# Optimization experiments

Measured on AMD Instinct MI355X. Metric: run time of the kernel, lower is better.

## Reference

```python
import jax, jax.numpy as jnp
import numpy as np

B, RSS_DIM, N_LED, LED_FEAT, HEAD_DIM = 1024, 12, 2048, 8, 64


def _mlp(x, W1, b1, W2, b2):
    # two-layer MLP with ReLU hidden
    return jax.nn.relu(x @ W1 + b1) @ W2 + b2


def setup_inputs() -> dict:
    key = jax.random.key(0)
    ks = jax.random.split(key, 16)
    s = lambda fan_in: 1.0 / np.sqrt(fan_in)
    inp = {
        "rss_t": jax.random.uniform(ks[0], (B, RSS_DIM, 1), jnp.float32),
        "led_features": jax.random.normal(ks[1], (B, N_LED, LED_FEAT), jnp.float32),
        "led_positions": jax.random.normal(ks[2], (B, N_LED, 3), jnp.float32),
        "prev_pos": jax.random.normal(ks[3], (B, 3), jnp.float32),
        "freq_mask": jax.random.randint(ks[4], (RSS_DIM, N_LED), 0, 2, jnp.int32),
        # intensity_gate: Linear(1,16) -> ReLU -> Linear(16,1) -> Sigmoid
        "Wg1": jax.random.normal(ks[5], (1, 16), jnp.float32) * s(1),
        "bg1": jnp.zeros((16,), jnp.float32),
        "Wg2": jax.random.normal(ks[6], (16, 1), jnp.float32) * s(16),
        "bg2": jnp.zeros((1,), jnp.float32),
        # query_proj: Linear(1,32) -> ReLU -> Linear(32,64)
        "Wq1": jax.random.normal(ks[7], (1, 32), jnp.float32) * s(1),
        "bq1": jnp.zeros((32,), jnp.float32),
        "Wq2": jax.random.normal(ks[8], (32, HEAD_DIM), jnp.float32) * s(32),
        "bq2": jnp.zeros((HEAD_DIM,), jnp.float32),
        # key_proj: Linear(led_feat+3, 32) -> ReLU -> Linear(32, 64)
        "Wk1": jax.random.normal(ks[9], (LED_FEAT + 3, 32), jnp.float32) * s(LED_FEAT + 3),
        "bk1": jnp.zeros((32,), jnp.float32),
        "Wk2": jax.random.normal(ks[10], (32, HEAD_DIM), jnp.float32) * s(32),
        "bk2": jnp.zeros((HEAD_DIM,), jnp.float32),
        "sigma": jnp.asarray(0.5, jnp.float32),
    }
    return inp


def reference(rss_t, led_features, led_positions, prev_pos, freq_mask,
              Wg1, bg1, Wg2, bg2, Wq1, bq1, Wq2, bq2, Wk1, bk1, Wk2, bk2, sigma):
    # gated intensity filter on RSS channels
    hard_mask = (rss_t > 0.5).astype(rss_t.dtype)              # [B, R, 1]
    soft_gate = jax.nn.sigmoid(_mlp(rss_t, Wg1, bg1, Wg2, bg2))  # [B, R, 1]
    intensity_weight = hard_mask * soft_gate                    # [B, R, 1]
    masked_rss = rss_t * intensity_weight

    Q = _mlp(masked_rss, Wq1, bq1, Wq2, bq2)                    # [B, R, D]
    led_input = jnp.concatenate([led_features, led_positions], axis=-1)  # [B, N, F+3]
    K = _mlp(led_input, Wk1, bk1, Wk2, bk2)                     # [B, N, D]

    attn_scores = jnp.einsum("brd,bnd->brn", Q, K)              # [B, R, N]

    # near-field distance bias from previous position
    dist_sq = jnp.sum((prev_pos[:, None, :] - led_positions) ** 2, axis=-1)  # [B, N]
    near_field_bias = -dist_sq[:, None, :] / (2.0 * sigma ** 2)  # broadcast to [B, R, N]
    attn_scores = attn_scores + near_field_bias

    # hard frequency mask then softmax over LEDs
    neg = jnp.finfo(attn_scores.dtype).min
    attn_scores = jnp.where(freq_mask[None, :, :] == 0, neg, attn_scores)
    attn_weights = jax.nn.softmax(attn_scores, axis=-1)
    return attn_weights, intensity_weight[..., 0]
```

## Files before the change

kernel.cpp:

```cpp
#include <hip/hip_runtime.h>
#include <math.h>
#include <float.h>

#define B_ 1024
#define R_ 12
#define N_ 2048

typedef float floatx4 __attribute__((ext_vector_type(4)));

__global__ void __launch_bounds__(1024) const_kernel(
    const float* __restrict__ Wq2, const float* __restrict__ bq2,
    const float* __restrict__ Wk2, const float* __restrict__ bk2,
    const float* __restrict__ Wk1, const float* __restrict__ bk1,
    float* __restrict__ Mmat, float* __restrict__ uvec,
    float* __restrict__ vvec, float* __restrict__ k0p,
    float* __restrict__ WkT)
{
    const int t = threadIdx.x;
    const int i = t >> 5, j = t & 31;
    float m = 0.0f;
    for (int d = 0; d < 64; d++) m += Wq2[i * 64 + d] * Wk2[j * 64 + d];
    Mmat[t] = m;
    if (t < 32) {
        float v = 0.0f;
        for (int d = 0; d < 64; d++) v += Wk2[t * 64 + d] * bq2[d];
        vvec[t] = v;
    } else if (t < 64) {
        float u = 0.0f;
        for (int d = 0; d < 64; d++) u += Wq2[(t - 32) * 64 + d] * bk2[d];
        uvec[t - 32] = u;
    } else if (t == 64) {
        float k = 0.0f;
        for (int d = 0; d < 64; d++) k += bq2[d] * bk2[d];
        k0p[0] = k;
    }
    if (t < 384) {
        const int jj = t / 12, e = t - jj * 12;
        WkT[t] = (e < 11) ? Wk1[e * 32 + jj] : bk1[jj];
    }
}

__global__ void __launch_bounds__(256) prep_kernel(
    const float* __restrict__ rss,
    const float* __restrict__ Wg1, const float* __restrict__ bg1,
    const float* __restrict__ Wg2, const float* __restrict__ bg2,
    const float* __restrict__ Wq1, const float* __restrict__ bq1,
    const float* __restrict__ Mmat, const float* __restrict__ uvec,
    const float* __restrict__ vvec, const float* __restrict__ k0p,
    const int*   __restrict__ mask,
    float* __restrict__ qpT,
    float* __restrict__ cc,
    int*   __restrict__ maskbits,
    float* __restrict__ inten_out)
{
    const int gt = blockIdx.x * 256 + threadIdx.x;

    if (gt < N_) {
        int bits = 0;
#pragma unroll
        for (int r = 0; r < R_; r++) bits |= (mask[r * N_ + gt] != 0) << r;
        maskbits[gt] = bits;
    }

    if (gt >= B_ * R_) return;
    const int b = gt / 12, r = gt - b * 12;

    const float x = rss[gt];
    const float hard = (x > 0.5f) ? 1.0f : 0.0f;

    float s2 = bg2[0];
#pragma unroll
    for (int i = 0; i < 16; i++)
        s2 += fmaxf(x * Wg1[i] + bg1[i], 0.0f) * Wg2[i];
    const float gate = 1.0f / (1.0f + __expf(-s2));
    const float iw = hard * gate;
    const float xm = x * iw;

    const floatx4* vv = reinterpret_cast<const floatx4*>(vvec);
    floatx4 Q0 = vv[0], Q1 = vv[1], Q2 = vv[2], Q3 = vv[3];
    floatx4 Q4 = vv[4], Q5 = vv[5], Q6 = vv[6], Q7 = vv[7];
    float c = k0p[0];

#pragma unroll
    for (int i = 0; i < 32; i++) {
        const float h = fmaxf(xm * Wq1[i] + bq1[i], 0.0f);
        const floatx4* mr = reinterpret_cast<const floatx4*>(Mmat + i * 32);
        Q0 += h * mr[0]; Q1 += h * mr[1]; Q2 += h * mr[2]; Q3 += h * mr[3];
        Q4 += h * mr[4]; Q5 += h * mr[5]; Q6 += h * mr[6]; Q7 += h * mr[7];
        c  += h * uvec[i];
    }

    float* qb = qpT + (size_t)b * 384 + r;
#define STQ(k)                          \
    qb[(4 * k + 0) * 12] = Q##k.x;      \
    qb[(4 * k + 1) * 12] = Q##k.y;      \
    qb[(4 * k + 2) * 12] = Q##k.z;      \
    qb[(4 * k + 3) * 12] = Q##k.w;
    STQ(0) STQ(1) STQ(2) STQ(3) STQ(4) STQ(5) STQ(6) STQ(7)
#undef STQ

    cc[gt] = c;
    inten_out[gt] = iw;
}

__global__ void __launch_bounds__(512, 2) main_kernel(
    const float* __restrict__ ledf,
    const float* __restrict__ ledp,
    const float* __restrict__ prevp,
    const int*   __restrict__ maskbits,
    const float* __restrict__ WkT,
    const float* __restrict__ qpT,
    const float* __restrict__ cc,
    const float* __restrict__ sigp,
    float* __restrict__ out)
{
    const int b = blockIdx.x;
    const int tid = threadIdx.x;
    const int lane = tid & 63;
    const int wave = tid >> 6;
    const int n0 = tid * 4;

    __shared__ float sW[32 * 12];
    __shared__ float sQ[32 * 12];
    __shared__ float red[8 * 12];

    if (tid < 384) {
        sW[tid] = WkT[tid];
        sQ[tid] = qpT[(size_t)b * 384 + tid];
    }

    const float* __restrict__ ccb = cc + b * 12;
    const float sig = sigp[0];
    const float nfc = -0.5f / (sig * sig);
    const float p0 = prevp[b * 3 + 0];
    const float p1 = prevp[b * 3 + 1];
    const float p2 = prevp[b * 3 + 2];

    const floatx4* pf = reinterpret_cast<const floatx4*>(ledf + ((size_t)b * N_ + n0) * 8);
    const floatx4* pp4 = reinterpret_cast<const floatx4*>(ledp + ((size_t)b * N_ + n0) * 3);
    const floatx4 F0 = pf[0], F1 = pf[1], F2 = pf[2], F3 = pf[3];
    const floatx4 F4 = pf[4], F5 = pf[5], F6 = pf[6], F7 = pf[7];
    const floatx4 pa = pp4[0], pb = pp4[1], pc = pp4[2];
    const int4 mb = *reinterpret_cast<const int4*>(maskbits + n0);

    const floatx4 X0 = {F0.x, F2.x, F4.x, F6.x};
    const floatx4 X1 = {F0.y, F2.y, F4.y, F6.y};
    const floatx4 X2 = {F0.z, F2.z, F4.z, F6.z};
    const floatx4 X3 = {F0.w, F2.w, F4.w, F6.w};
    const floatx4 X4 = {F1.x, F3.x, F5.x, F7.x};
    const floatx4 X5 = {F1.y, F3.y, F5.y, F7.y};
    const floatx4 X6 = {F1.z, F3.z, F5.z, F7.z};
    const floatx4 X7 = {F1.w, F3.w, F5.w, F7.w};
    const floatx4 X8 = {pa.x, pa.w, pb.z, pc.y};
    const floatx4 X9 = {pa.y, pb.x, pb.w, pc.z};
    const floatx4 X10 = {pa.z, pb.y, pc.x, pc.w};

    const floatx4 DX = p0 - X8, DY = p1 - X9, DZ = p2 - X10;
    const floatx4 BIAS = nfc * (DX * DX + DY * DY + DZ * DZ);

#define FOR_R(OP) OP(0) OP(1) OP(2) OP(3) OP(4) OP(5) OP(6) OP(7) OP(8) OP(9) OP(10) OP(11)
#define INIT_R(r) floatx4 A##r = BIAS + ccb[r];
    FOR_R(INIT_R)

    __syncthreads();

#pragma unroll 4
    for (int j = 0; j < 32; j++) {
        const floatx4 w0 = *reinterpret_cast<const floatx4*>(&sW[j * 12]);
        const floatx4 w1 = *reinterpret_cast<const floatx4*>(&sW[j * 12 + 4]);
        const floatx4 w2 = *reinterpret_cast<const floatx4*>(&sW[j * 12 + 8]);
        const floatx4 q0 = *reinterpret_cast<const floatx4*>(&sQ[j * 12]);
        const floatx4 q1 = *reinterpret_cast<const floatx4*>(&sQ[j * 12 + 4]);
        const floatx4 q2 = *reinterpret_cast<const floatx4*>(&sQ[j * 12 + 8]);

        floatx4 H = {w2.w, w2.w, w2.w, w2.w};
        H += X0 * w0.x;  H += X1 * w0.y;  H += X2 * w0.z;  H += X3 * w0.w;
        H += X4 * w1.x;  H += X5 * w1.y;  H += X6 * w1.z;  H += X7 * w1.w;
        H += X8 * w2.x;  H += X9 * w2.y;  H += X10 * w2.z;
        H.x = fmaxf(H.x, 0.0f);
        H.y = fmaxf(H.y, 0.0f);
        H.z = fmaxf(H.z, 0.0f);
        H.w = fmaxf(H.w, 0.0f);

        A0 += H * q0.x;  A1 += H * q0.y;  A2  += H * q0.z;  A3  += H * q0.w;
        A4 += H * q1.x;  A5 += H * q1.y;  A6  += H * q1.z;  A7  += H * q1.w;
        A8 += H * q2.x;  A9 += H * q2.y;  A10 += H * q2.z;  A11 += H * q2.w;
    }

#define MASK_R(r)                                      \
    A##r.x = ((mb.x >> r) & 1) ? A##r.x : -FLT_MAX;    \
    A##r.y = ((mb.y >> r) & 1) ? A##r.y : -FLT_MAX;    \
    A##r.z = ((mb.z >> r) & 1) ? A##r.z : -FLT_MAX;    \
    A##r.w = ((mb.w >> r) & 1) ? A##r.w : -FLT_MAX;
    FOR_R(MASK_R)

#define WMAX_R(r) {                                                     \
    float v = fmaxf(fmaxf(A##r.x, A##r.y), fmaxf(A##r.z, A##r.w));      \
    _Pragma("unroll")                                                   \
    for (int off = 32; off >= 1; off >>= 1) v = fmaxf(v, __shfl_xor(v, off)); \
    if (lane == 0) red[wave * 12 + r] = v; }
    FOR_R(WMAX_R)
    __syncthreads();
#define FMAX_R(r) float M##r = red[r];                                  \
    { _Pragma("unroll")                                                 \
      for (int w = 1; w < 8; w++) M##r = fmaxf(M##r, red[w * 12 + r]); }
    FOR_R(FMAX_R)
    __syncthreads();

#define EXP_R(r) {                                                      \
    A##r.x = __expf(A##r.x - M##r); A##r.y = __expf(A##r.y - M##r);     \
    A##r.z = __expf(A##r.z - M##r); A##r.w = __expf(A##r.w - M##r);     \
    float v = (A##r.x + A##r.y) + (A##r.z + A##r.w);                    \
    _Pragma("unroll")                                                   \
    for (int off = 32; off >= 1; off >>= 1) v += __shfl_xor(v, off);    \
    if (lane == 0) red[wave * 12 + r] = v; }
    FOR_R(EXP_R)
    __syncthreads();
#define FSUM_R(r) float S##r = red[r];                                  \
    { _Pragma("unroll")                                                 \
      for (int w = 1; w < 8; w++) S##r += red[w * 12 + r]; }            \
    S##r = 1.0f / S##r;
    FOR_R(FSUM_R)

    float* outp = out + (size_t)b * R_ * N_ + n0;
#define STORE_R(r) {                                                    \
    floatx4 v = A##r * S##r;                                            \
    __builtin_nontemporal_store(v, reinterpret_cast<floatx4*>(outp + (size_t)r * N_)); }
    FOR_R(STORE_R)
}

extern "C" void kernel_launch(void* const* d_in, const int* in_sizes, int n_in,
                              void* d_out, int out_size, void* d_ws, size_t ws_size,
                              hipStream_t stream) {
    const float* rss  = (const float*)d_in[0];
    const float* ledf = (const float*)d_in[1];
    const float* ledp = (const float*)d_in[2];
    const float* prevp= (const float*)d_in[3];
    const int*   mask = (const int*)  d_in[4];
    const float* Wg1  = (const float*)d_in[5];
    const float* bg1  = (const float*)d_in[6];
    const float* Wg2  = (const float*)d_in[7];
    const float* bg2  = (const float*)d_in[8];
    const float* Wq1  = (const float*)d_in[9];
    const float* bq1  = (const float*)d_in[10];
    const float* Wq2  = (const float*)d_in[11];
    const float* bq2  = (const float*)d_in[12];
    const float* Wk1  = (const float*)d_in[13];
    const float* bk1  = (const float*)d_in[14];
    const float* Wk2  = (const float*)d_in[15];
    const float* bk2  = (const float*)d_in[16];
    const float* sigp = (const float*)d_in[17];

    float* out = (float*)d_out;
    float* inten = out + (size_t)B_ * R_ * N_;

    float* qpT      = (float*)d_ws;
    float* cc       = qpT + (size_t)B_ * 384;
    int*   maskbits = (int*)(cc + B_ * R_);
    float* Mmat     = (float*)(maskbits + N_);
    float* uvec     = Mmat + 1024;
    float* vvec     = uvec + 32;
    float* k0p      = vvec + 32;
    float* WkT      = k0p + 4;

    const_kernel<<<1, 1024, 0, stream>>>(Wq2, bq2, Wk2, bk2, Wk1, bk1,
                                         Mmat, uvec, vvec, k0p, WkT);

    prep_kernel<<<(B_ * R_ + 255) / 256, 256, 0, stream>>>(
        rss, Wg1, bg1, Wg2, bg2, Wq1, bq1,
        Mmat, uvec, vvec, k0p, mask, qpT, cc, maskbits, inten);

    main_kernel<<<B_, 512, 0, stream>>>(
        ledf, ledp, prevp, maskbits, WkT, qpT, cc, sigp, out);
}
```

Measured before the change: 293.4 us.

## Process two batches per block with 8 LEDs per thread and prefetch

The main kernel now uses 512 blocks of 256 threads. Each block handles batches b and b+512, and each thread covers 8 LEDs instead of 4. The second batch's LED feature and position loads are issued before the first batch's softmax and stores, so that global-load latency hides behind reduction work. In exchange, far fewer waves are resident, register pressure is much higher, and memory-latency hiding now depends on the explicit prefetch rather than occupancy.

```diff
diff --git a/kernel.cpp b/kernel.cpp
--- a/kernel.cpp
+++ b/kernel.cpp
@@ -92,10 +92,10 @@
 
     float* qb = qpT + (size_t)b * 384 + r;
 #define STQ(k)                          \
-    qb[(4 * k + 0) * 12] = Q##k.x;      \
-    qb[(4 * k + 1) * 12] = Q##k.y;      \
-    qb[(4 * k + 2) * 12] = Q##k.z;      \
-    qb[(4 * k + 3) * 12] = Q##k.w;
+    qb[(4 * k + 0) * 12] = Q##k .x;     \
+    qb[(4 * k + 1) * 12] = Q##k .y;     \
+    qb[(4 * k + 2) * 12] = Q##k .z;     \
+    qb[(4 * k + 3) * 12] = Q##k .w;
     STQ(0) STQ(1) STQ(2) STQ(3) STQ(4) STQ(5) STQ(6) STQ(7)
 #undef STQ
 
@@ -103,7 +103,121 @@
     inten_out[gt] = iw;
 }
 
-__global__ void __launch_bounds__(512, 2) main_kernel(
+#define FOR_R(OP) OP(0) OP(1) OP(2) OP(3) OP(4) OP(5) OP(6) OP(7) OP(8) OP(9) OP(10) OP(11)
+#define FOR_R2(OP, X) OP(0,X) OP(1,X) OP(2,X) OP(3,X) OP(4,X) OP(5,X) OP(6,X) OP(7,X) OP(8,X) OP(9,X) OP(10,X) OP(11,X)
+
+#define TRANS_BIAS(O, F, P, PX, PY, PZ)                                 \
+    const floatx4 O##A0 = {F##0 .x, F##2 .x, F##4 .x, F##6 .x};         \
+    const floatx4 O##A1 = {F##0 .y, F##2 .y, F##4 .y, F##6 .y};         \
+    const floatx4 O##A2 = {F##0 .z, F##2 .z, F##4 .z, F##6 .z};         \
+    const floatx4 O##A3 = {F##0 .w, F##2 .w, F##4 .w, F##6 .w};         \
+    const floatx4 O##A4 = {F##1 .x, F##3 .x, F##5 .x, F##7 .x};         \
+    const floatx4 O##A5 = {F##1 .y, F##3 .y, F##5 .y, F##7 .y};         \
+    const floatx4 O##A6 = {F##1 .z, F##3 .z, F##5 .z, F##7 .z};         \
+    const floatx4 O##A7 = {F##1 .w, F##3 .w, F##5 .w, F##7 .w};         \
+    const floatx4 O##A8 = {P##0 .x, P##0 .w, P##1 .z, P##2 .y};         \
+    const floatx4 O##A9 = {P##0 .y, P##1 .x, P##1 .w, P##2 .z};         \
+    const floatx4 O##A10 = {P##0 .z, P##1 .y, P##2 .x, P##2 .w};        \
+    const floatx4 O##B0 = {F##8 .x, F##10 .x, F##12 .x, F##14 .x};      \
+    const floatx4 O##B1 = {F##8 .y, F##10 .y, F##12 .y, F##14 .y};      \
+    const floatx4 O##B2 = {F##8 .z, F##10 .z, F##12 .z, F##14 .z};      \
+    const floatx4 O##B3 = {F##8 .w, F##10 .w, F##12 .w, F##14 .w};      \
+    const floatx4 O##B4 = {F##9 .x, F##11 .x, F##13 .x, F##15 .x};      \
+    const floatx4 O##B5 = {F##9 .y, F##11 .y, F##13 .y, F##15 .y};      \
+    const floatx4 O##B6 = {F##9 .z, F##11 .z, F##13 .z, F##15 .z};      \
+    const floatx4 O##B7 = {F##9 .w, F##11 .w, F##13 .w, F##15 .w};      \
+    const floatx4 O##B8 = {P##3 .x, P##3 .w, P##4 .z, P##5 .y};         \
+    const floatx4 O##B9 = {P##3 .y, P##4 .x, P##4 .w, P##5 .z};         \
+    const floatx4 O##B10 = {P##3 .z, P##4 .y, P##5 .x, P##5 .w};        \
+    const floatx4 O##DXA = PX - O##A8, O##DYA = PY - O##A9, O##DZA = PZ - O##A10; \
+    const floatx4 O##BIA = nfc * (O##DXA * O##DXA + O##DYA * O##DYA + O##DZA * O##DZA); \
+    const floatx4 O##DXB = PX - O##B8, O##DYB = PY - O##B9, O##DZB = PZ - O##B10; \
+    const floatx4 O##BIB = nfc * (O##DXB * O##DXB + O##DYB * O##DYB + O##DZB * O##DZB);
+
+#define JLOOP(PA, PB, SQ)                                               \
+    _Pragma("unroll 2")                                                 \
+    for (int j = 0; j < 32; j++) {                                      \
+        const floatx4 w0 = *reinterpret_cast<const floatx4*>(&sW[j * 12]); \
+        const floatx4 w1 = *reinterpret_cast<const floatx4*>(&sW[j * 12 + 4]); \
+        const floatx4 w2 = *reinterpret_cast<const floatx4*>(&sW[j * 12 + 8]); \
+        const floatx4 q0 = *reinterpret_cast<const floatx4*>(&SQ[j * 12]); \
+        const floatx4 q1 = *reinterpret_cast<const floatx4*>(&SQ[j * 12 + 4]); \
+        const floatx4 q2 = *reinterpret_cast<const floatx4*>(&SQ[j * 12 + 8]); \
+        floatx4 HA = {w2.w, w2.w, w2.w, w2.w};                          \
+        floatx4 HB = HA;                                                \
+        HA += PA##0 * w0.x;  HB += PB##0 * w0.x;                        \
+        HA += PA##1 * w0.y;  HB += PB##1 * w0.y;                        \
+        HA += PA##2 * w0.z;  HB += PB##2 * w0.z;                        \
+        HA += PA##3 * w0.w;  HB += PB##3 * w0.w;                        \
+        HA += PA##4 * w1.x;  HB += PB##4 * w1.x;                        \
+        HA += PA##5 * w1.y;  HB += PB##5 * w1.y;                        \
+        HA += PA##6 * w1.z;  HB += PB##6 * w1.z;                        \
+        HA += PA##7 * w1.w;  HB += PB##7 * w1.w;                        \
+        HA += PA##8 * w2.x;  HB += PB##8 * w2.x;                        \
+        HA += PA##9 * w2.y;  HB += PB##9 * w2.y;                        \
+        HA += PA##10 * w2.z; HB += PB##10 * w2.z;                       \
+        HA.x = fmaxf(HA.x, 0.0f); HA.y = fmaxf(HA.y, 0.0f);             \
+        HA.z = fmaxf(HA.z, 0.0f); HA.w = fmaxf(HA.w, 0.0f);             \
+        HB.x = fmaxf(HB.x, 0.0f); HB.y = fmaxf(HB.y, 0.0f);             \
+        HB.z = fmaxf(HB.z, 0.0f); HB.w = fmaxf(HB.w, 0.0f);             \
+        AA0 += HA * q0.x;  AB0 += HB * q0.x;                            \
+        AA1 += HA * q0.y;  AB1 += HB * q0.y;                            \
+        AA2 += HA * q0.z;  AB2 += HB * q0.z;                            \
+        AA3 += HA * q0.w;  AB3 += HB * q0.w;                            \
+        AA4 += HA * q1.x;  AB4 += HB * q1.x;                            \
+        AA5 += HA * q1.y;  AB5 += HB * q1.y;                            \
+        AA6 += HA * q1.z;  AB6 += HB * q1.z;                            \
+        AA7 += HA * q1.w;  AB7 += HB * q1.w;                            \
+        AA8 += HA * q2.x;  AB8 += HB * q2.x;                            \
+        AA9 += HA * q2.y;  AB9 += HB * q2.y;                            \
+        AA10 += HA * q2.z; AB10 += HB * q2.z;                           \
+        AA11 += HA * q2.w; AB11 += HB * q2.w;                           \
+    }
+
+#define MASK_R(r)                                            \
+    AA##r .x = ((mbA.x >> r) & 1) ? AA##r .x : -FLT_MAX;     \
+    AA##r .y = ((mbA.y >> r) & 1) ? AA##r .y : -FLT_MAX;     \
+    AA##r .z = ((mbA.z >> r) & 1) ? AA##r .z : -FLT_MAX;     \
+    AA##r .w = ((mbA.w >> r) & 1) ? AA##r .w : -FLT_MAX;     \
+    AB##r .x = ((mbB.x >> r) & 1) ? AB##r .x : -FLT_MAX;     \
+    AB##r .y = ((mbB.y >> r) & 1) ? AB##r .y : -FLT_MAX;     \
+    AB##r .z = ((mbB.z >> r) & 1) ? AB##r .z : -FLT_MAX;     \
+    AB##r .w = ((mbB.w >> r) & 1) ? AB##r .w : -FLT_MAX;
+
+#define WMAX2_R(r, RM) {                                                \
+    float v = fmaxf(fmaxf(fmaxf(AA##r .x, AA##r .y), fmaxf(AA##r .z, AA##r .w)), \
+                    fmaxf(fmaxf(AB##r .x, AB##r .y), fmaxf(AB##r .z, AB##r .w))); \
+    _Pragma("unroll")                                                   \
+    for (int off = 32; off >= 1; off >>= 1) v = fmaxf(v, __shfl_xor(v, off)); \
+    if (lane == 0) RM[wave * 12 + r] = v; }
+
+#define FMAX2_R(r, RM) float M##r = RM[r];                              \
+    { _Pragma("unroll")                                                 \
+      for (int w = 1; w < 4; w++) M##r = fmaxf(M##r, RM[w * 12 + r]); }
+
+#define EXP2_R(r, RS) {                                                 \
+    AA##r .x = __expf(AA##r .x - M##r); AA##r .y = __expf(AA##r .y - M##r); \
+    AA##r .z = __expf(AA##r .z - M##r); AA##r .w = __expf(AA##r .w - M##r); \
+    AB##r .x = __expf(AB##r .x - M##r); AB##r .y = __expf(AB##r .y - M##r); \
+    AB##r .z = __expf(AB##r .z - M##r); AB##r .w = __expf(AB##r .w - M##r); \
+    float v = ((AA##r .x + AA##r .y) + (AA##r .z + AA##r .w))           \
+            + ((AB##r .x + AB##r .y) + (AB##r .z + AB##r .w));          \
+    _Pragma("unroll")                                                   \
+    for (int off = 32; off >= 1; off >>= 1) v += __shfl_xor(v, off);    \
+    if (lane == 0) RS[wave * 12 + r] = v; }
+
+#define FSUM2_R(r, RS) float S##r = RS[r];                              \
+    { _Pragma("unroll")                                                 \
+      for (int w = 1; w < 4; w++) S##r += RS[w * 12 + r]; }             \
+    S##r = 1.0f / S##r;
+
+#define STORE2_R(r, OUTP) {                                             \
+    floatx4 vA = AA##r * S##r;                                          \
+    floatx4 vB = AB##r * S##r;                                          \
+    __builtin_nontemporal_store(vA, reinterpret_cast<floatx4*>(OUTP + (size_t)r * N_)); \
+    __builtin_nontemporal_store(vB, reinterpret_cast<floatx4*>(OUTP + (size_t)r * N_ + 4)); }
+
+__global__ void __launch_bounds__(256, 1) main_kernel(
     const float* __restrict__ ledf,
     const float* __restrict__ ledp,
     const float* __restrict__ prevp,
@@ -114,119 +228,88 @@
     const float* __restrict__ sigp,
     float* __restrict__ out)
 {
-    const int b = blockIdx.x;
+    const int bid = blockIdx.x;
+    const int b0 = bid, b1 = bid + 512;
     const int tid = threadIdx.x;
     const int lane = tid & 63;
     const int wave = tid >> 6;
-    const int n0 = tid * 4;
-
-    __shared__ float sW[32 * 12];
-    __shared__ float sQ[32 * 12];
-    __shared__ float red[8 * 12];
-
-    if (tid < 384) {
-        sW[tid] = WkT[tid];
-        sQ[tid] = qpT[(size_t)b * 384 + tid];
-    }
-
-    const float* __restrict__ ccb = cc + b * 12;
+    const int n0 = tid * 8;
+
+    __shared__ float sW[384], sQ0[384], sQ1[384];
+    __shared__ float redM0[48], redS0[48], redM1[48], redS1[48];
+
+    for (int i = tid; i < 384; i += 256) {
+        sW[i] = WkT[i];
+        sQ0[i] = qpT[(size_t)b0 * 384 + i];
+        sQ1[i] = qpT[(size_t)b1 * 384 + i];
+    }
+
     const float sig = sigp[0];
     const float nfc = -0.5f / (sig * sig);
-    const float p0 = prevp[b * 3 + 0];
-    const float p1 = prevp[b * 3 + 1];
-    const float p2 = prevp[b * 3 + 2];
-
-    const floatx4* pf = reinterpret_cast<const floatx4*>(ledf + ((size_t)b * N_ + n0) * 8);
-    const floatx4* pp4 = reinterpret_cast<const floatx4*>(ledp + ((size_t)b * N_ + n0) * 3);
-    const floatx4 F0 = pf[0], F1 = pf[1], F2 = pf[2], F3 = pf[3];
-    const floatx4 F4 = pf[4], F5 = pf[5], F6 = pf[6], F7 = pf[7];
-    const floatx4 pa = pp4[0], pb = pp4[1], pc = pp4[2];
-    const int4 mb = *reinterpret_cast<const int4*>(maskbits + n0);
-
-    const floatx4 X0 = {F0.x, F2.x, F4.x, F6.x};
-    const floatx4 X1 = {F0.y, F2.y, F4.y, F6.y};
-    const floatx4 X2 = {F0.z, F2.z, F4.z, F6.z};
-    const floatx4 X3 = {F0.w, F2.w, F4.w, F6.w};
-    const floatx4 X4 = {F1.x, F3.x, F5.x, F7.x};
-    const floatx4 X5 = {F1.y, F3.y, F5.y, F7.y};
-    const floatx4 X6 = {F1.z, F3.z, F5.z, F7.z};
-    const floatx4 X7 = {F1.w, F3.w, F5.w, F7.w};
-    const floatx4 X8 = {pa.x, pa.w, pb.z, pc.y};
-    const floatx4 X9 = {pa.y, pb.x, pb.w, pc.z};
-    const floatx4 X10 = {pa.z, pb.y, pc.x, pc.w};
-
-    const floatx4 DX = p0 - X8, DY = p1 - X9, DZ = p2 - X10;
-    const floatx4 BIAS = nfc * (DX * DX + DY * DY + DZ * DZ);
-
-#define FOR_R(OP) OP(0) OP(1) OP(2) OP(3) OP(4) OP(5) OP(6) OP(7) OP(8) OP(9) OP(10) OP(11)
-#define INIT_R(r) floatx4 A##r = BIAS + ccb[r];
+    const float p0a = prevp[b0 * 3 + 0], p1a = prevp[b0 * 3 + 1], p2a = prevp[b0 * 3 + 2];
+    const float p0b = prevp[b1 * 3 + 0], p1b = prevp[b1 * 3 + 1], p2b = prevp[b1 * 3 + 2];
+    const float* __restrict__ ccb0 = cc + b0 * 12;
+    const float* __restrict__ ccb1 = cc + b1 * 12;
+
+    const floatx4* pf  = reinterpret_cast<const floatx4*>(ledf + ((size_t)b0 * N_ + n0) * 8);
+    const floatx4* pp4 = reinterpret_cast<const floatx4*>(ledp + ((size_t)b0 * N_ + n0) * 3);
+    const int4*    pm  = reinterpret_cast<const int4*>(maskbits + n0);
+    const floatx4 F0 = pf[0],  F1 = pf[1],  F2 = pf[2],  F3 = pf[3];
+    const floatx4 F4 = pf[4],  F5 = pf[5],  F6 = pf[6],  F7 = pf[7];
+    const floatx4 F8 = pf[8],  F9 = pf[9],  F10 = pf[10], F11 = pf[11];
+    const floatx4 F12 = pf[12], F13 = pf[13], F14 = pf[14], F15 = pf[15];
+    const floatx4 pa0 = pp4[0], pa1 = pp4[1], pa2 = pp4[2];
+    const floatx4 pa3 = pp4[3], pa4 = pp4[4], pa5 = pp4[5];
+    const int4 mbA = pm[0], mbB = pm[1];
+
+    TRANS_BIAS(X, F, pa, p0a, p1a, p2a)
+
+#define INIT_R(r) floatx4 AA##r = XBIA + ccb0[r]; floatx4 AB##r = XBIB + ccb0[r];
     FOR_R(INIT_R)
 
     __syncthreads();
 
-#pragma unroll 4
-    for (int j = 0; j < 32; j++) {
-        const floatx4 w0 = *reinterpret_cast<const floatx4*>(&sW[j * 12]);
-        const floatx4 w1 = *reinterpret_cast<const floatx4*>(&sW[j * 12 + 4]);
-        const floatx4 w2 = *reinterpret_cast<const floatx4*>(&sW[j * 12 + 8]);
-        const floatx4 q0 = *reinterpret_cast<const floatx4*>(&sQ[j * 12]);
-        const floatx4 q1 = *reinterpret_cast<const floatx4*>(&sQ[j * 12 + 4]);
-        const floatx4 q2 = *reinterpret_cast<const floatx4*>(&sQ[j * 12 + 8]);
-
-        floatx4 H = {w2.w, w2.w, w2.w, w2.w};
-        H += X0 * w0.x;  H += X1 * w0.y;  H += X2 * w0.z;  H += X3 * w0.w;
-        H += X4 * w1.x;  H += X5 * w1.y;  H += X6 * w1.z;  H += X7 * w1.w;
-        H += X8 * w2.x;  H += X9 * w2.y;  H += X10 * w2.z;
-        H.x = fmaxf(H.x, 0.0f);
-        H.y = fmaxf(H.y, 0.0f);
-        H.z = fmaxf(H.z, 0.0f);
-        H.w = fmaxf(H.w, 0.0f);
-
-        A0 += H * q0.x;  A1 += H * q0.y;  A2  += H * q0.z;  A3  += H * q0.w;
-        A4 += H * q1.x;  A5 += H * q1.y;  A6  += H * q1.z;  A7  += H * q1.w;
-        A8 += H * q2.x;  A9 += H * q2.y;  A10 += H * q2.z;  A11 += H * q2.w;
-    }
-
-#define MASK_R(r)                                      \
-    A##r.x = ((mb.x >> r) & 1) ? A##r.x : -FLT_MAX;    \
-    A##r.y = ((mb.y >> r) & 1) ? A##r.y : -FLT_MAX;    \
-    A##r.z = ((mb.z >> r) & 1) ? A##r.z : -FLT_MAX;    \
-    A##r.w = ((mb.w >> r) & 1) ? A##r.w : -FLT_MAX;
+    JLOOP(XA, XB, sQ0)
     FOR_R(MASK_R)
 
-#define WMAX_R(r) {                                                     \
-    float v = fmaxf(fmaxf(A##r.x, A##r.y), fmaxf(A##r.z, A##r.w));      \
-    _Pragma("unroll")                                                   \
-    for (int off = 32; off >= 1; off >>= 1) v = fmaxf(v, __shfl_xor(v, off)); \
-    if (lane == 0) red[wave * 12 + r] = v; }
-    FOR_R(WMAX_R)
-    __syncthreads();
-#define FMAX_R(r) float M##r = red[r];                                  \
-    { _Pragma("unroll")                                                 \
-      for (int w = 1; w < 8; w++) M##r = fmaxf(M##r, red[w * 12 + r]); }
-    FOR_R(FMAX_R)
-    __syncthreads();
-
-#define EXP_R(r) {                                                      \
-    A##r.x = __expf(A##r.x - M##r); A##r.y = __expf(A##r.y - M##r);     \
-    A##r.z = __expf(A##r.z - M##r); A##r.w = __expf(A##r.w - M##r);     \
-    float v = (A##r.x + A##r.y) + (A##r.z + A##r.w);                    \
-    _Pragma("unroll")                                                   \
-    for (int off = 32; off >= 1; off >>= 1) v += __shfl_xor(v, off);    \
-    if (lane == 0) red[wave * 12 + r] = v; }
-    FOR_R(EXP_R)
-    __syncthreads();
-#define FSUM_R(r) float S##r = red[r];                                  \
-    { _Pragma("unroll")                                                 \
-      for (int w = 1; w < 8; w++) S##r += red[w * 12 + r]; }            \
-    S##r = 1.0f / S##r;
-    FOR_R(FSUM_R)
-
-    float* outp = out + (size_t)b * R_ * N_ + n0;
-#define STORE_R(r) {                                                    \
-    floatx4 v = A##r * S##r;                                            \
-    __builtin_nontemporal_store(v, reinterpret_cast<floatx4*>(outp + (size_t)r * N_)); }
-    FOR_R(STORE_R)
+    const floatx4* gf  = reinterpret_cast<const floatx4*>(ledf + ((size_t)b1 * N_ + n0) * 8);
+    const floatx4* gp4 = reinterpret_cast<const floatx4*>(ledp + ((size_t)b1 * N_ + n0) * 3);
+    const floatx4 G0 = gf[0],  G1 = gf[1],  G2 = gf[2],  G3 = gf[3];
+    const floatx4 G4 = gf[4],  G5 = gf[5],  G6 = gf[6],  G7 = gf[7];
+    const floatx4 G8 = gf[8],  G9 = gf[9],  G10 = gf[10], G11 = gf[11];
+    const floatx4 G12 = gf[12], G13 = gf[13], G14 = gf[14], G15 = gf[15];
+    const floatx4 ga0 = gp4[0], ga1 = gp4[1], ga2 = gp4[2];
+    const floatx4 ga3 = gp4[3], ga4 = gp4[4], ga5 = gp4[5];
+
+    {
+        FOR_R2(WMAX2_R, redM0)
+        __syncthreads();
+        FOR_R2(FMAX2_R, redM0)
+        FOR_R2(EXP2_R, redS0)
+        __syncthreads();
+        FOR_R2(FSUM2_R, redS0)
+        float* outp = out + (size_t)b0 * R_ * N_ + n0;
+        FOR_R2(STORE2_R, outp)
+    }
+
+    TRANS_BIAS(Y, G, ga, p0b, p1b, p2b)
+
+#define REINIT_R(r) AA##r = YBIA + ccb1[r]; AB##r = YBIB + ccb1[r];
+    FOR_R(REINIT_R)
+
+    JLOOP(YA, YB, sQ1)
+    FOR_R(MASK_R)
+
+    {
+        FOR_R2(WMAX2_R, redM1)
+        __syncthreads();
+        FOR_R2(FMAX2_R, redM1)
+        FOR_R2(EXP2_R, redS1)
+        __syncthreads();
+        FOR_R2(FSUM2_R, redS1)
+        float* outp = out + (size_t)b1 * R_ * N_ + n0;
+        FOR_R2(STORE2_R, outp)
+    }
 }
 
 extern "C" void kernel_launch(void* const* d_in, const int* in_sizes, int n_in,
@@ -270,6 +353,6 @@
         rss, Wg1, bg1, Wg2, bg2, Wq1, bq1,
         Mmat, uvec, vvec, k0p, mask, qpT, cc, maskbits, inten);
 
-    main_kernel<<<B_, 512, 0, stream>>>(
+    main_kernel<<<512, 256, 0, stream>>>(
         ledf, ledp, prevp, maskbits, WkT, qpT, cc, sigp, out);
 }
```

After: 293.4 us. Within noise of the previous version (+0.0%).
